# Kernel optimization log

Measured on AMD Instinct MI355X. Metric: run time of the kernel, lower is better.

## Reference

```python
import jax, jax.numpy as jnp
import numpy as np
import math

B, A, M, NC = 16, 8400, 64, 80
TOPK, ALPHA, BETA, EPS = 10, 0.5, 6.0, 1e-9


def _make_anchors():
    pts = []
    for s in (8, 16, 32):
        n = 640 // s
        yv, xv = jnp.meshgrid(jnp.arange(n, dtype=jnp.float32), jnp.arange(n, dtype=jnp.float32), indexing='ij')
        pts.append(jnp.stack([(xv + 0.5) * s, (yv + 0.5) * s], axis=-1).reshape(-1, 2))
    return jnp.concatenate(pts, axis=0)  # [8400, 2]


def setup_inputs() -> dict:
    key = jax.random.key(0)
    k = jax.random.split(key, 8)
    pd_scores = jax.random.uniform(k[0], (B, A, NC), dtype=jnp.float32)
    anc_points = _make_anchors()  # [A,2]
    # predicted boxes: jittered anchor centers with random sizes (xyxy)
    wh = jax.random.uniform(k[1], (B, A, 2), dtype=jnp.float32) * 80.0 + 8.0
    ctr = anc_points[None] + jax.random.normal(k[2], (B, A, 2), dtype=jnp.float32) * 4.0
    pd_bboxes = jnp.concatenate([ctr - wh / 2, ctr + wh / 2], axis=-1)
    # gt boxes: centers/sizes inside a 640px image (xyxy)
    gctr = jax.random.uniform(k[3], (B, M, 2), dtype=jnp.float32) * 560.0 + 40.0
    gwh = jax.random.uniform(k[4], (B, M, 2), dtype=jnp.float32) * 180.0 + 20.0
    gt_bboxes = jnp.concatenate([gctr - gwh / 2, gctr + gwh / 2], axis=-1)
    gt_labels = jax.random.randint(k[5], (B, M, 1), 0, NC, dtype=jnp.int32)
    # variable number of valid gts per image
    counts = jax.random.randint(k[6], (B, 1, 1), 8, M, dtype=jnp.int32)
    mask_gt = (jnp.arange(M)[None, :, None] < counts).astype(jnp.float32)
    return {"pd_scores": pd_scores, "pd_bboxes": pd_bboxes, "anc_points": anc_points,
            "gt_labels": gt_labels, "gt_bboxes": gt_bboxes, "mask_gt": mask_gt}


def _ciou(box1, box2, eps=1e-7):
    b1x1, b1y1, b1x2, b1y2 = jnp.split(box1, 4, axis=-1)
    b2x1, b2y1, b2x2, b2y2 = jnp.split(box2, 4, axis=-1)
    w1, h1 = b1x2 - b1x1, b1y2 - b1y1 + eps
    w2, h2 = b2x2 - b2x1, b2y2 - b2y1 + eps
    inter = (jnp.clip(jnp.minimum(b1x2, b2x2) - jnp.maximum(b1x1, b2x1), 0)
             * jnp.clip(jnp.minimum(b1y2, b2y2) - jnp.maximum(b1y1, b2y1), 0))
    union = w1 * h1 + w2 * h2 - inter + eps
    iou = inter / union
    cw = jnp.maximum(b1x2, b2x2) - jnp.minimum(b1x1, b2x1)
    ch = jnp.maximum(b1y2, b2y2) - jnp.minimum(b1y1, b2y1)
    c2 = cw ** 2 + ch ** 2 + eps
    rho2 = ((b2x1 + b2x2 - b1x1 - b1x2) ** 2 + (b2y1 + b2y2 - b1y1 - b1y2) ** 2) / 4.0
    v = (4.0 / math.pi ** 2) * (jnp.arctan(w2 / h2) - jnp.arctan(w1 / h1)) ** 2
    alpha = jax.lax.stop_gradient(v / (v - iou + (1.0 + eps)))
    return iou - (rho2 / c2 + v * alpha)


def reference(pd_scores, pd_bboxes, anc_points, gt_labels, gt_bboxes, mask_gt):
    b, a, nc = pd_scores.shape
    m = gt_bboxes.shape[1]
    lt, rb = gt_bboxes[..., :2], gt_bboxes[..., 2:]  # [B,M,2]
    # anchor-in-gt test: deltas [B,M,A,4]
    deltas = jnp.concatenate([anc_points[None, None] - lt[:, :, None],
                              rb[:, :, None] - anc_points[None, None]], axis=-1)
    mask_in_gts = deltas.min(axis=-1) > EPS  # [B,M,A]
    mask_pos_gt = mask_in_gts & (mask_gt > 0)  # [B,M,A] (mask_gt [B,M,1] broadcasts)
    # per-gt class score: pd_scores[b, :, gt_labels[b, m]] -> [B,M,A]
    scoresT = jnp.swapaxes(pd_scores, 1, 2)  # [B,nc,A]
    idx = jnp.broadcast_to(gt_labels.astype(jnp.int32), (b, m, a))
    bbox_scores = jnp.where(mask_pos_gt, jnp.take_along_axis(scoresT, idx, axis=1), 0.0)
    iou = _ciou(gt_bboxes[:, :, None, :], pd_bboxes[:, None, :, :])[..., 0]  # [B,M,A]
    overlaps = jnp.where(mask_pos_gt, jnp.clip(iou, 0.0), 0.0)
    align_metric = bbox_scores ** ALPHA * overlaps ** BETA
    # top-k candidate anchors per gt
    kk = min(TOPK, a)
    topk_metrics, topk_idx = jax.lax.top_k(align_metric, kk)  # [B,M,k]
    keep = (topk_metrics > EPS) & jnp.take_along_axis(mask_pos_gt, topk_idx, axis=-1)
    topk_idx = jnp.where(keep, topk_idx, 0)  # masked indices -> 0, as in original
    bi = jnp.arange(b)[:, None, None]
    mi = jnp.arange(m)[None, :, None]
    cnt = jnp.zeros((b, m, a), jnp.int32).at[bi, mi, topk_idx].add(1)
    mask_top_k = jnp.minimum(cnt, 1).astype(align_metric.dtype)
    mask_pos = (mask_top_k * mask_in_gts.astype(align_metric.dtype)
                * mask_pos_gt.astype(align_metric.dtype))  # [B,M,A]
    fg_mask = mask_pos.sum(axis=1)  # [B,A]
    # anchors claimed by multiple gts -> assign to max-overlap gt
    mask_multi = fg_mask[:, None, :] > 1  # [B,1,A]
    is_max = jax.nn.one_hot(overlaps.argmax(axis=1), m, axis=1, dtype=mask_pos.dtype)
    mask_pos = jnp.where(mask_multi, is_max, mask_pos)
    fg_mask = mask_pos.sum(axis=1)
    target_gt_idx = mask_pos.argmax(axis=1)  # [B,A]
    target_labels = jnp.maximum(
        jnp.take_along_axis(gt_labels[..., 0].astype(jnp.int32), target_gt_idx, axis=1), 0)
    target_bboxes = jnp.take_along_axis(gt_bboxes, target_gt_idx[..., None], axis=1)  # [B,A,4]
    target_scores = jax.nn.one_hot(target_labels, NC, dtype=jnp.int32)
    target_scores = jnp.where(fg_mask[..., None] > 0, target_scores, 0)
    align_metric = align_metric * mask_pos
    pos_align = align_metric.max(axis=-1, keepdims=True)  # [B,M,1]
    pos_overlaps = (overlaps * mask_pos).max(axis=-1, keepdims=True)
    norm = (align_metric * pos_overlaps / (pos_align + EPS)).max(axis=1)[..., None]  # [B,A,1]
    target_scores = target_scores.astype(norm.dtype) * norm
    return target_bboxes, target_scores, fg_mask > 0
```

## Files before the change

kernel.cpp:

```cpp
#include <hip/hip_runtime.h>
#include <math.h>

#define NB 16
#define NA 8400
#define NM 64
#define NCLS 80
#define KTOP 10
#define EPS_T 1e-9f
#define CEPS 1e-7f
#define KPL 20

__device__ __forceinline__ float ciou_clip(float4 g, float4 p)
{
    float w1 = g.z - g.x, h1 = g.w - g.y + CEPS;
    float w2 = p.z - p.x, h2 = p.w - p.y + CEPS;
    float iw = fmaxf(fminf(g.z, p.z) - fmaxf(g.x, p.x), 0.f);
    float ih = fmaxf(fminf(g.w, p.w) - fmaxf(g.y, p.y), 0.f);
    float inter = iw * ih;
    float uni = w1 * h1 + w2 * h2 - inter + CEPS;
    float iou = inter / uni;
    float cw = fmaxf(g.z, p.z) - fminf(g.x, p.x);
    float ch = fmaxf(g.w, p.w) - fminf(g.y, p.y);
    float c2 = cw * cw + ch * ch + CEPS;
    float dx = p.x + p.z - g.x - g.z;
    float dy = p.y + p.w - g.y - g.w;
    float rho2 = (dx * dx + dy * dy) * 0.25f;
    float dat = atanf(w2 / h2) - atanf(w1 / h1);
    float v = (4.f / (float)(M_PI * M_PI)) * dat * dat;
    float alpha = v / (v - iou + (1.f + CEPS));
    return fmaxf(iou - (rho2 / c2 + v * alpha), 0.f);
}

__device__ __forceinline__ float pow6(float x) { float x2 = x * x; return x2 * x2 * x2; }

__device__ __forceinline__ bool inbox(float ax, float ay, float4 g)
{
    return fminf(fminf(ax - g.x, ay - g.y), fminf(g.z - ax, g.w - ay)) > EPS_T;
}

__global__ __launch_bounds__(64) void k1_fused(
    const float* __restrict__ pd_scores, const float* __restrict__ pd_bboxes,
    const int* __restrict__ gt_labels, const float* __restrict__ gt_bboxes,
    const float* __restrict__ mask_gt,
    unsigned int* __restrict__ count, int* __restrict__ claim_m,
    float* __restrict__ claim_align, float* __restrict__ claim_ovl)
{
    int lane = threadIdx.x;
    int m = blockIdx.x, b = blockIdx.y;
    int gi = b * NM + m;
    float mg = mask_gt[gi];
    if (mg <= 0.f) return;

    float4 g = *(const float4*)(gt_bboxes + (size_t)gi * 4);
    int lbl = gt_labels[gi];
    const float4* pd4 = (const float4*)(pd_bboxes + (size_t)b * NA * 4);
    const float* sc_b = pd_scores + (size_t)b * NA * NCLS + lbl;

    int c0[3], r0[3], wL[3], cnt[3];
    int nL[3] = {80, 40, 20};
    int baseL[3] = {0, 6400, 8000};
    float sL[3] = {8.f, 16.f, 32.f};
    #pragma unroll
    for (int l = 0; l < 3; ++l) {
        float s = sL[l]; int n = nL[l];
        int cA = (int)floorf(g.x / s - 0.5f);
        int cB = (int)ceilf(g.z / s - 0.5f);
        int rA = (int)floorf(g.y / s - 0.5f);
        int rB = (int)ceilf(g.w / s - 0.5f);
        cA = cA < 0 ? 0 : cA;  rA = rA < 0 ? 0 : rA;
        cB = cB > n - 1 ? n - 1 : cB;  rB = rB > n - 1 ? n - 1 : rB;
        int w = cB - cA + 1;  if (w < 0) w = 0;
        int h = rB - rA + 1;  if (h < 0) h = 0;
        c0[l] = cA; r0[l] = rA; wL[l] = w; cnt[l] = w * h;
    }
    int t01 = cnt[0] + cnt[1];
    int T = t01 + cnt[2];
    if (T > KPL * 64) T = KPL * 64;

    unsigned long long keys[KPL];
    #pragma unroll
    for (int sidx = 0; sidx < KPL; ++sidx) {
        keys[sidx] = 0ull;
        int i = lane + sidx * 64;
        if (i < T) {
            int l, j;
            if (i < cnt[0])      { l = 0; j = i; }
            else if (i < t01)    { l = 1; j = i - cnt[0]; }
            else                 { l = 2; j = i - t01; }
            int w = wL[l];
            int rr = j / w, cc = j - rr * w;
            int c = c0[l] + cc, r = r0[l] + rr;
            float s = sL[l];
            float ax = ((float)c + 0.5f) * s;
            float ay = ((float)r + 0.5f) * s;
            int a = baseL[l] + r * nL[l] + c;
            if (inbox(ax, ay, g)) {
                float ov = ciou_clip(g, pd4[a]);
                if (ov > 0.f) {
                    float am = sqrtf(sc_b[(size_t)a * NCLS]) * pow6(ov);
                    if (am > 0.f)
                        keys[sidx] = ((unsigned long long)__float_as_uint(am) << 32)
                                   | (unsigned)(NA - a);
                }
            }
        }
    }

    int nwin = 0, ndisc = 0;
    int wa = -1;
    for (int k = 0; k < KTOP; ++k) {
        unsigned long long best = 0ull;
        #pragma unroll
        for (int j = 0; j < KPL; ++j) if (keys[j] > best) best = keys[j];
        for (int off = 32; off; off >>= 1) {
            unsigned long long o = __shfl_xor(best, off);
            if (o > best) best = o;
        }
        if (best == 0ull) { ndisc += KTOP - k; break; }
        #pragma unroll
        for (int j = 0; j < KPL; ++j) if (keys[j] == best) keys[j] = 0ull;
        float val = __uint_as_float((unsigned)(best >> 32));
        int a = NA - (int)(best & 0xffffffffull);
        if (val > EPS_T) {
            if (lane == nwin) wa = a;
            ++nwin;
        } else {
            ++ndisc;
        }
    }

    if (lane < nwin) {
        int a = wa;
        float ov = ciou_clip(g, pd4[a]);
        float am = 0.f;
        if (ov > 0.f) am = sqrtf(sc_b[(size_t)a * NCLS]) * pow6(ov);
        size_t col = (size_t)b * NA + a;
        atomicAdd(&count[col], 1u);
        claim_m[col] = m;
        claim_align[col] = am;
        claim_ovl[col] = ov;
    }

    if (ndisc > 0) {
        unsigned long long dup = __ballot(lane < nwin && wa == 0);
        if (lane == 0 && dup == 0ull && inbox(4.f, 4.f, g)) {
            float ov = ciou_clip(g, pd4[0]);
            float am = 0.f;
            if (ov > 0.f) am = sqrtf(sc_b[0]) * pow6(ov);
            size_t col = (size_t)b * NA;
            atomicAdd(&count[col], 1u);
            claim_m[col] = m;
            claim_align[col] = am;
            claim_ovl[col] = ov;
        }
    }
}

__global__ __launch_bounds__(256) void k3_resolve(
    const unsigned int* __restrict__ count, const int* __restrict__ claim_m,
    const float* __restrict__ claim_align, const float* __restrict__ claim_ovl,
    const float* __restrict__ pd_scores, const float* __restrict__ pd_bboxes,
    const float* __restrict__ anc, const int* __restrict__ gt_labels,
    const float* __restrict__ gt_bboxes, const float* __restrict__ mask_gt,
    float* __restrict__ out_bbox, float* __restrict__ out_fg,
    int* __restrict__ col_tgt, float* __restrict__ col_av,
    unsigned int* __restrict__ pos_align, unsigned int* __restrict__ pos_ovl)
{
    int idx = blockIdx.x * 256 + threadIdx.x;
    if (idx >= NB * NA) return;
    int b = idx / NA, a = idx - b * NA;
    unsigned int c = count[idx];
    int tgt = -1; float av = 0.f, ov = 0.f;
    if (c == 1u) {
        tgt = claim_m[idx]; av = claim_align[idx]; ov = claim_ovl[idx];
    } else if (c > 1u) {
        float2 ap = ((const float2*)anc)[a];
        float4 p = *(const float4*)(pd_bboxes + ((size_t)b * NA + a) * 4);
        float bv = -1.f; int bm = 0;
        for (int mm = 0; mm < NM; ++mm) {
            int gi = b * NM + mm;
            float4 gg = *(const float4*)(gt_bboxes + (size_t)gi * 4);
            float mgv = mask_gt[gi];
            float din = fminf(fminf(ap.x - gg.x, ap.y - gg.y),
                              fminf(gg.z - ap.x, gg.w - ap.y));
            float ovm = 0.f;
            if (din > EPS_T && mgv > 0.f) ovm = ciou_clip(gg, p);
            if (ovm > bv) { bv = ovm; bm = mm; }
        }
        tgt = bm; ov = bv;
        if (ov > 0.f) {
            int lbl = gt_labels[b * NM + bm];
            float sc = pd_scores[((size_t)b * NA + a) * NCLS + lbl];
            av = sqrtf(sc) * pow6(ov);
        }
    }
    int fg = (c > 0u);
    int safet = tgt < 0 ? 0 : tgt;
    float4 gt = *(const float4*)(gt_bboxes + ((size_t)b * NM + safet) * 4);
    *(float4*)(out_bbox + (size_t)idx * 4) = gt;
    out_fg[idx] = fg ? 1.f : 0.f;
    col_tgt[idx] = fg ? tgt : -1;
    col_av[idx] = av;
    if (fg) {
        atomicMax(&pos_align[b * NM + tgt], __float_as_uint(av));
        atomicMax(&pos_ovl[b * NM + tgt], __float_as_uint(ov));
    }
}

__global__ __launch_bounds__(256) void k4_scores(
    const int* __restrict__ col_tgt, const float* __restrict__ col_av,
    const unsigned int* __restrict__ pos_align, const unsigned int* __restrict__ pos_ovl,
    const int* __restrict__ gt_labels, float* __restrict__ out_scores)
{
    __shared__ float s_ratio[NM];
    __shared__ float s_norm[256];
    __shared__ int s_lbl[256];
    int t = threadIdx.x;
    int b = blockIdx.y;
    int a0 = blockIdx.x * 256;
    if (t < NM) {
        float pa = __uint_as_float(pos_align[b * NM + t]);
        float po = __uint_as_float(pos_ovl[b * NM + t]);
        s_ratio[t] = po / (pa + EPS_T);
    }
    __syncthreads();
    int a = a0 + t;
    float nrm = 0.f; int lbl = -1;
    if (a < NA) {
        int tgt = col_tgt[(size_t)b * NA + a];
        if (tgt >= 0) {
            nrm = col_av[(size_t)b * NA + a] * s_ratio[tgt];
            lbl = gt_labels[b * NM + tgt];
            if (lbl < 0) lbl = 0;
        }
    }
    s_norm[t] = nrm;
    s_lbl[t] = lbl;
    __syncthreads();
    int n_a = NA - a0; if (n_a > 256) n_a = 256;
    size_t obase = ((size_t)b * NA + a0) * NCLS;
    for (int i = t; i < n_a * NCLS; i += 256) {
        int al = i / NCLS, c = i - al * NCLS;
        out_scores[obase + i] = (c == s_lbl[al]) ? s_norm[al] : 0.f;
    }
}

extern "C" void kernel_launch(void* const* d_in, const int* in_sizes, int n_in,
                              void* d_out, int out_size, void* d_ws, size_t ws_size,
                              hipStream_t stream)
{
    const float* pd_scores = (const float*)d_in[0];
    const float* pd_bboxes = (const float*)d_in[1];
    const float* anc       = (const float*)d_in[2];
    const int*   gt_labels = (const int*)d_in[3];
    const float* gt_bboxes = (const float*)d_in[4];
    const float* mask_gt   = (const float*)d_in[5];

    size_t szBA = (size_t)NB * NA;
    unsigned int* count = (unsigned int*)d_ws;
    int*   claim_m     = (int*)(count + szBA);
    float* claim_align = (float*)(claim_m + szBA);
    float* claim_ovl   = claim_align + szBA;
    int*   col_tgt     = (int*)(claim_ovl + szBA);
    float* col_av      = (float*)(col_tgt + szBA);
    unsigned int* pos_align = (unsigned int*)(col_av + szBA);
    unsigned int* pos_ovl   = pos_align + NB * NM;

    float* out_bbox   = (float*)d_out;
    float* out_scores = out_bbox + (size_t)NB * NA * 4;
    float* out_fg     = out_scores + (size_t)NB * NA * NCLS;

    hipMemsetAsync(count, 0, szBA * sizeof(unsigned int), stream);
    hipMemsetAsync(pos_align, 0, 2 * NB * NM * sizeof(unsigned int), stream);

    k1_fused<<<dim3(NM, NB), 64, 0, stream>>>(pd_scores, pd_bboxes, gt_labels,
                                              gt_bboxes, mask_gt,
                                              count, claim_m, claim_align, claim_ovl);
    k3_resolve<<<(int)((szBA + 255) / 256), 256, 0, stream>>>(
        count, claim_m, claim_align, claim_ovl, pd_scores, pd_bboxes, anc,
        gt_labels, gt_bboxes, mask_gt, out_bbox, out_fg, col_tgt, col_av,
        pos_align, pos_ovl);
    k4_scores<<<dim3((NA + 255) / 256, NB), 256, 0, stream>>>(
        col_tgt, col_av, pos_align, pos_ovl, gt_labels, out_scores);
}
```

Measured before the change: 152.3 us.

## Split per-GT top-k across four waves, cache GT data in LDS, vectorize score stores

After: 133.4 us. 12.5% less time.

```diff
diff --git a/kernel.cpp b/kernel.cpp
--- a/kernel.cpp
+++ b/kernel.cpp
@@ -8,7 +8,7 @@
 #define KTOP 10
 #define EPS_T 1e-9f
 #define CEPS 1e-7f
-#define KPL 20
+#define KPL 5
 
 __device__ __forceinline__ float ciou_clip(float4 g, float4 p)
 {
@@ -38,14 +38,17 @@
     return fminf(fminf(ax - g.x, ay - g.y), fminf(g.z - ax, g.w - ay)) > EPS_T;
 }
 
-__global__ __launch_bounds__(64) void k1_fused(
+__global__ __launch_bounds__(256) void k1_fused(
     const float* __restrict__ pd_scores, const float* __restrict__ pd_bboxes,
     const int* __restrict__ gt_labels, const float* __restrict__ gt_bboxes,
     const float* __restrict__ mask_gt,
     unsigned int* __restrict__ count, int* __restrict__ claim_m,
     float* __restrict__ claim_align, float* __restrict__ claim_ovl)
 {
-    int lane = threadIdx.x;
+    __shared__ unsigned long long lds_keys[4][KTOP];
+
+    int t = threadIdx.x;
+    int wv = t >> 6, lane = t & 63;
     int m = blockIdx.x, b = blockIdx.y;
     int gi = b * NM + m;
     float mg = mask_gt[gi];
@@ -75,13 +78,13 @@
     }
     int t01 = cnt[0] + cnt[1];
     int T = t01 + cnt[2];
-    if (T > KPL * 64) T = KPL * 64;
+    if (T > KPL * 256) T = KPL * 256;
 
     unsigned long long keys[KPL];
     #pragma unroll
     for (int sidx = 0; sidx < KPL; ++sidx) {
         keys[sidx] = 0ull;
-        int i = lane + sidx * 64;
+        int i = sidx * 256 + wv * 64 + lane;
         if (i < T) {
             int l, j;
             if (i < cnt[0])      { l = 0; j = i; }
@@ -106,8 +109,7 @@
         }
     }
 
-    int nwin = 0, ndisc = 0;
-    int wa = -1;
+    unsigned long long mykey = 0ull;
     for (int k = 0; k < KTOP; ++k) {
         unsigned long long best = 0ull;
         #pragma unroll
@@ -116,88 +118,114 @@
             unsigned long long o = __shfl_xor(best, off);
             if (o > best) best = o;
         }
-        if (best == 0ull) { ndisc += KTOP - k; break; }
+        if (best == 0ull) break;
         #pragma unroll
         for (int j = 0; j < KPL; ++j) if (keys[j] == best) keys[j] = 0ull;
-        float val = __uint_as_float((unsigned)(best >> 32));
-        int a = NA - (int)(best & 0xffffffffull);
-        if (val > EPS_T) {
-            if (lane == nwin) wa = a;
-            ++nwin;
-        } else {
-            ++ndisc;
-        }
-    }
-
-    if (lane < nwin) {
-        int a = wa;
+        if (lane == k) mykey = best;
+    }
+    if (lane < KTOP) lds_keys[wv][lane] = mykey;
+    __syncthreads();
+
+    if (wv != 0) return;
+    unsigned long long fk = 0ull;
+    if (lane < 4 * KTOP) fk = lds_keys[lane / KTOP][lane % KTOP];
+
+    unsigned long long winkey = 0ull;
+    for (int k = 0; k < KTOP; ++k) {
+        unsigned long long best = fk;
+        for (int off = 32; off; off >>= 1) {
+            unsigned long long o = __shfl_xor(best, off);
+            if (o > best) best = o;
+        }
+        if (best == 0ull) break;
+        if (fk == best) fk = 0ull;
+        if (lane == k) winkey = best;
+    }
+
+    float val = __uint_as_float((unsigned)(winkey >> 32));
+    int a = NA - (int)(winkey & 0xffffffffull);
+    bool slot = (lane < KTOP);
+    bool poswin = slot && (winkey != 0ull) && (val > EPS_T);
+    unsigned long long disc = __ballot(slot && !poswin);
+    unsigned long long dup0 = __ballot(poswin && a == 0);
+
+    if (poswin) {
         float ov = ciou_clip(g, pd4[a]);
+        size_t col = (size_t)b * NA + a;
+        atomicAdd(&count[col], 1u);
+        claim_m[col] = m;
+        claim_align[col] = val;
+        claim_ovl[col] = ov;
+    }
+    if (disc != 0ull && dup0 == 0ull && lane == 0 && inbox(4.f, 4.f, g)) {
+        float ov = ciou_clip(g, pd4[0]);
         float am = 0.f;
-        if (ov > 0.f) am = sqrtf(sc_b[(size_t)a * NCLS]) * pow6(ov);
-        size_t col = (size_t)b * NA + a;
+        if (ov > 0.f) am = sqrtf(sc_b[0]) * pow6(ov);
+        size_t col = (size_t)b * NA;
         atomicAdd(&count[col], 1u);
         claim_m[col] = m;
         claim_align[col] = am;
         claim_ovl[col] = ov;
     }
-
-    if (ndisc > 0) {
-        unsigned long long dup = __ballot(lane < nwin && wa == 0);
-        if (lane == 0 && dup == 0ull && inbox(4.f, 4.f, g)) {
-            float ov = ciou_clip(g, pd4[0]);
-            float am = 0.f;
-            if (ov > 0.f) am = sqrtf(sc_b[0]) * pow6(ov);
-            size_t col = (size_t)b * NA;
-            atomicAdd(&count[col], 1u);
-            claim_m[col] = m;
-            claim_align[col] = am;
-            claim_ovl[col] = ov;
-        }
-    }
 }
 
 __global__ __launch_bounds__(256) void k3_resolve(
     const unsigned int* __restrict__ count, const int* __restrict__ claim_m,
     const float* __restrict__ claim_align, const float* __restrict__ claim_ovl,
     const float* __restrict__ pd_scores, const float* __restrict__ pd_bboxes,
-    const float* __restrict__ anc, const int* __restrict__ gt_labels,
-    const float* __restrict__ gt_bboxes, const float* __restrict__ mask_gt,
+    const int* __restrict__ gt_labels, const float* __restrict__ gt_bboxes,
+    const float* __restrict__ mask_gt,
     float* __restrict__ out_bbox, float* __restrict__ out_fg,
     int* __restrict__ col_tgt, float* __restrict__ col_av,
     unsigned int* __restrict__ pos_align, unsigned int* __restrict__ pos_ovl)
 {
-    int idx = blockIdx.x * 256 + threadIdx.x;
-    if (idx >= NB * NA) return;
-    int b = idx / NA, a = idx - b * NA;
+    __shared__ float4 s_g[NM];
+    __shared__ float s_mg[NM];
+    __shared__ int s_lb[NM];
+    int t = threadIdx.x;
+    int b = blockIdx.y;
+    if (t < NM) {
+        int gi = b * NM + t;
+        s_g[t] = *(const float4*)(gt_bboxes + (size_t)gi * 4);
+        s_mg[t] = mask_gt[gi];
+        s_lb[t] = gt_labels[gi];
+    }
+    __syncthreads();
+
+    int a = blockIdx.x * 256 + t;
+    if (a >= NA) return;
+    size_t idx = (size_t)b * NA + a;
     unsigned int c = count[idx];
     int tgt = -1; float av = 0.f, ov = 0.f;
     if (c == 1u) {
         tgt = claim_m[idx]; av = claim_align[idx]; ov = claim_ovl[idx];
     } else if (c > 1u) {
-        float2 ap = ((const float2*)anc)[a];
-        float4 p = *(const float4*)(pd_bboxes + ((size_t)b * NA + a) * 4);
+        int l, j, n; float s;
+        if (a < 6400)      { l = 0; j = a;        n = 80; s = 8.f; }
+        else if (a < 8000) { l = 1; j = a - 6400; n = 40; s = 16.f; }
+        else               { l = 2; j = a - 8000; n = 20; s = 32.f; }
+        int rr = j / n, cc = j - rr * n;
+        float ax = ((float)cc + 0.5f) * s, ay = ((float)rr + 0.5f) * s;
+        float4 p = *(const float4*)(pd_bboxes + idx * 4);
         float bv = -1.f; int bm = 0;
         for (int mm = 0; mm < NM; ++mm) {
-            int gi = b * NM + mm;
-            float4 gg = *(const float4*)(gt_bboxes + (size_t)gi * 4);
-            float mgv = mask_gt[gi];
-            float din = fminf(fminf(ap.x - gg.x, ap.y - gg.y),
-                              fminf(gg.z - ap.x, gg.w - ap.y));
+            float4 gg = s_g[mm];
+            float din = fminf(fminf(ax - gg.x, ay - gg.y),
+                              fminf(gg.z - ax, gg.w - ay));
             float ovm = 0.f;
-            if (din > EPS_T && mgv > 0.f) ovm = ciou_clip(gg, p);
+            if (din > EPS_T && s_mg[mm] > 0.f) ovm = ciou_clip(gg, p);
             if (ovm > bv) { bv = ovm; bm = mm; }
         }
         tgt = bm; ov = bv;
         if (ov > 0.f) {
-            int lbl = gt_labels[b * NM + bm];
-            float sc = pd_scores[((size_t)b * NA + a) * NCLS + lbl];
+            float sc = pd_scores[idx * NCLS + s_lb[bm]];
             av = sqrtf(sc) * pow6(ov);
         }
     }
     int fg = (c > 0u);
     int safet = tgt < 0 ? 0 : tgt;
-    float4 gt = *(const float4*)(gt_bboxes + ((size_t)b * NM + safet) * 4);
-    *(float4*)(out_bbox + (size_t)idx * 4) = gt;
+    float4 gt = s_g[safet];
+    *(float4*)(out_bbox + idx * 4) = gt;
     out_fg[idx] = fg ? 1.f : 0.f;
     col_tgt[idx] = fg ? tgt : -1;
     col_av[idx] = av;
@@ -238,10 +266,18 @@
     s_lbl[t] = lbl;
     __syncthreads();
     int n_a = NA - a0; if (n_a > 256) n_a = 256;
-    size_t obase = ((size_t)b * NA + a0) * NCLS;
-    for (int i = t; i < n_a * NCLS; i += 256) {
-        int al = i / NCLS, c = i - al * NCLS;
-        out_scores[obase + i] = (c == s_lbl[al]) ? s_norm[al] : 0.f;
+    float4* out4 = (float4*)(out_scores + ((size_t)b * NA + a0) * NCLS);
+    int n4 = n_a * (NCLS / 4);
+    for (int i4 = t; i4 < n4; i4 += 256) {
+        int al = i4 / (NCLS / 4);
+        int cb = (i4 - al * (NCLS / 4)) * 4;
+        float nv = s_norm[al]; int lb = s_lbl[al];
+        float4 v;
+        v.x = (cb == lb) ? nv : 0.f;
+        v.y = (cb + 1 == lb) ? nv : 0.f;
+        v.z = (cb + 2 == lb) ? nv : 0.f;
+        v.w = (cb + 3 == lb) ? nv : 0.f;
+        out4[i4] = v;
     }
 }
 
@@ -251,33 +287,31 @@
 {
     const float* pd_scores = (const float*)d_in[0];
     const float* pd_bboxes = (const float*)d_in[1];
-    const float* anc       = (const float*)d_in[2];
     const int*   gt_labels = (const int*)d_in[3];
     const float* gt_bboxes = (const float*)d_in[4];
     const float* mask_gt   = (const float*)d_in[5];
 
     size_t szBA = (size_t)NB * NA;
-    unsigned int* count = (unsigned int*)d_ws;
-    int*   claim_m     = (int*)(count + szBA);
+    unsigned int* count     = (unsigned int*)d_ws;
+    unsigned int* pos_align = count + szBA;
+    unsigned int* pos_ovl   = pos_align + NB * NM;
+    int*   claim_m     = (int*)(pos_ovl + NB * NM);
     float* claim_align = (float*)(claim_m + szBA);
     float* claim_ovl   = claim_align + szBA;
     int*   col_tgt     = (int*)(claim_ovl + szBA);
     float* col_av      = (float*)(col_tgt + szBA);
-    unsigned int* pos_align = (unsigned int*)(col_av + szBA);
-    unsigned int* pos_ovl   = pos_align + NB * NM;
 
     float* out_bbox   = (float*)d_out;
     float* out_scores = out_bbox + (size_t)NB * NA * 4;
     float* out_fg     = out_scores + (size_t)NB * NA * NCLS;
 
-    hipMemsetAsync(count, 0, szBA * sizeof(unsigned int), stream);
-    hipMemsetAsync(pos_align, 0, 2 * NB * NM * sizeof(unsigned int), stream);
-
-    k1_fused<<<dim3(NM, NB), 64, 0, stream>>>(pd_scores, pd_bboxes, gt_labels,
-                                              gt_bboxes, mask_gt,
-                                              count, claim_m, claim_align, claim_ovl);
-    k3_resolve<<<(int)((szBA + 255) / 256), 256, 0, stream>>>(
-        count, claim_m, claim_align, claim_ovl, pd_scores, pd_bboxes, anc,
+    hipMemsetAsync(count, 0, (szBA + 2 * NB * NM) * sizeof(unsigned int), stream);
+
+    k1_fused<<<dim3(NM, NB), 256, 0, stream>>>(pd_scores, pd_bboxes, gt_labels,
+                                               gt_bboxes, mask_gt,
+                                               count, claim_m, claim_align, claim_ovl);
+    k3_resolve<<<dim3((NA + 255) / 256, NB), 256, 0, stream>>>(
+        count, claim_m, claim_align, claim_ovl, pd_scores, pd_bboxes,
         gt_labels, gt_bboxes, mask_gt, out_bbox, out_fg, col_tgt, col_av,
         pos_align, pos_ovl);
     k4_scores<<<dim3((NA + 255) / 256, NB), 256, 0, stream>>>(
```
